# Performance work log

Hardware: AMD Instinct MI355X
Metric: run time of the kernel (lower is better)

The kernel has to match this reference:

```python
import jax, jax.numpy as jnp
import numpy as np

NEG = -1e9


def setup_inputs() -> dict:
    key = jax.random.key(0)
    kq, kk, kv, ke = jax.random.split(key, 4)
    B, H, S, D = 4, 16, 2048, 64
    q = jax.random.normal(kq, (B, H, S, D), dtype=jnp.float32)
    k = jax.random.normal(kk, (B, H, S, D), dtype=jnp.float32)
    v = jax.random.normal(kv, (B, H, S, D), dtype=jnp.float32)
    event_length = jax.random.randint(ke, (B,), 0, S, dtype=jnp.int32)
    return {"q": q, "k": k, "v": v, "event_length": event_length}


def reference(q, k, v, event_length):
    B, H, S, D = q.shape
    scale = jnp.sqrt(jnp.asarray(D, dtype=jnp.float32))
    # [b,h,s,q] scores
    scores = jnp.einsum('bhsd,bhqd->bhsq', q, k) / scale
    idx = jnp.arange(S)
    el = event_length[:, None]  # [B,1]
    valid = idx[None, :] < el   # [B,S]
    # mask[b,s,q] = valid[b,s] & valid[b,q]; broadcast over heads
    mask = (valid[:, None, :, None] & valid[:, None, None, :])  # [B,1,S,S]
    scores = jnp.where(mask, scores, NEG)
    attn = jax.nn.softmax(scores, axis=-1)
    # dropout p=0.0 (eval): identity
    out = jnp.einsum('bhsq,bhqd->bhsd', attn, v)
    return out
```

## Files before the change

kernel.cpp:

```cpp
#include <hip/hip_runtime.h>
#include <hip/hip_bf16.h>


#define SQ 2048
#define DH 64
#define NBH 64
#define TK 64
#define NTILE 32
#define TILE_B 8192
#define LDE 72
#define LVP 68

typedef __attribute__((ext_vector_type(4))) float f32x4;
typedef __attribute__((ext_vector_type(8))) short bf16x8;
typedef __attribute__((ext_vector_type(4))) unsigned int u32x4;
typedef __attribute__((ext_vector_type(2))) unsigned int u32x2;

__device__ __forceinline__ unsigned int pk2(float lo, float hi) {
    __hip_bfloat162 h = __float22bfloat162_rn(float2{lo, hi});
    union { __hip_bfloat162 h; unsigned int u; } c; c.h = h;
    return c.u;
}

__device__ __forceinline__ float bfu16_to_f(unsigned short s) {
    union { unsigned int u; float f; } c; c.u = ((unsigned int)s) << 16;
    return c.f;
}


__global__ __launch_bounds__(256)
void convkv(const float* __restrict__ K, const float* __restrict__ V,
            const int* __restrict__ EL, float* __restrict__ MV,
            char* __restrict__ Kbt, char* __restrict__ Vbt) {
    const int bh = blockIdx.x >> 5;
    const int kt = blockIdx.x & 31;
    const int k0 = kt * TK;
    const int el = EL[bh >> 4];
    const int t = threadIdx.x;
    const int r  = t >> 2;
    const int dc = t & 3;

    __shared__ short LV[64][LVP];

    {
        const float* vp = V + ((size_t)bh * SQ + k0 + r) * DH + dc * 16;
        f32x4 a = *(const f32x4*)vp;
        f32x4 b = *(const f32x4*)(vp + 4);
        f32x4 c2 = *(const f32x4*)(vp + 8);
        f32x4 d2 = *(const f32x4*)(vp + 12);
        u32x4 w0, w1;
        w0[0] = pk2(a[0], a[1]);  w0[1] = pk2(a[2], a[3]);
        w0[2] = pk2(b[0], b[1]);  w0[3] = pk2(b[2], b[3]);
        w1[0] = pk2(c2[0], c2[1]); w1[1] = pk2(c2[2], c2[3]);
        w1[2] = pk2(d2[0], d2[1]); w1[3] = pk2(d2[2], d2[3]);
        *(u32x4*)&LV[r][dc * 16]     = w0;
        *(u32x4*)&LV[r][dc * 16 + 8] = w1;
    }

    if (k0 < el) {
        const float* kp = K + ((size_t)bh * SQ + k0 + r) * DH + dc * 16;
        f32x4 a = *(const f32x4*)kp;
        f32x4 b = *(const f32x4*)(kp + 4);
        f32x4 c2 = *(const f32x4*)(kp + 8);
        f32x4 d2 = *(const f32x4*)(kp + 12);
        u32x4 w0, w1;
        w0[0] = pk2(a[0], a[1]);  w0[1] = pk2(a[2], a[3]);
        w0[2] = pk2(b[0], b[1]);  w0[3] = pk2(b[2], b[3]);
        w1[0] = pk2(c2[0], c2[1]); w1[1] = pk2(c2[2], c2[3]);
        w1[2] = pk2(d2[0], d2[1]); w1[3] = pk2(d2[2], d2[3]);
        char* kb = Kbt + (size_t)(bh * NTILE + kt) * TILE_B;
        const int fi  = (r >> 4) * 2 + (dc >> 1);
        const int qd0 = (dc & 1) * 2;
        char* d0 = kb + fi * 1024 + qd0 * 256 + (r & 15) * 16;
        *(u32x4*)d0         = w0;
        *(u32x4*)(d0 + 256) = w1;
    }

    __syncthreads();

    const int dd  = t >> 2;
    const int seg = t & 3;
    float msum = 0.f;
    unsigned int wv[8];
    #pragma unroll
    for (int i = 0; i < 8; ++i) {
        const int pos = seg * 16 + 2 * i;
        const int key = (pos & ~31) | ((pos & 4) << 2) | ((pos & 24) >> 1) | (pos & 3);
        const unsigned short s0 = (unsigned short)LV[key][dd];
        const unsigned short s1 = (unsigned short)LV[key + 1][dd];
        msum += bfu16_to_f(s0) + bfu16_to_f(s1);
        wv[i] = (unsigned int)s0 | ((unsigned int)s1 << 16);
    }
    msum += __shfl_xor(msum, 1);
    msum += __shfl_xor(msum, 2);
    if (seg == 0) atomicAdd(&MV[bh * DH + dd], msum * (1.0f / (float)SQ));

    if (k0 < el) {
        char* vbb = Vbt + (size_t)(bh * NTILE + kt) * TILE_B;
        const int fi  = (seg >> 1) * 4 + (dd >> 4);
        const int qd0 = (seg & 1) * 2;
        char* d0 = vbb + fi * 1024 + qd0 * 256 + (dd & 15) * 16;
        u32x4 o0 = {wv[0], wv[1], wv[2], wv[3]};
        u32x4 o1 = {wv[4], wv[5], wv[6], wv[7]};
        *(u32x4*)d0         = o0;
        *(u32x4*)(d0 + 256) = o1;
    }
}

__global__ __launch_bounds__(256, 3)
void flash8(const float* __restrict__ Q, const int* __restrict__ EL,
            const float* __restrict__ MV, float* __restrict__ O,
            const char* __restrict__ Kbt, const char* __restrict__ Vbt,
            int* __restrict__ ticket) {
    const int t = threadIdx.x;

    {
        const int bh0 = blockIdx.x & (NBH - 1);
        const int qb0 = (blockIdx.x >> 6) * 128;
        const int el32b = (EL[bh0 >> 4] + 31) & ~31;
        if (qb0 + 127 >= el32b) {
            float* Op = O + (size_t)bh0 * SQ * DH;
            const int c16 = t & 15, r0 = t >> 4;
            f32x4 mv = *(const f32x4*)(MV + bh0 * DH + c16 * 4);
            #pragma unroll
            for (int i = 0; i < 8; ++i) {
                const int row = qb0 + r0 + i * 16;
                if (row >= el32b)
                    *(f32x4*)(Op + (size_t)row * DH + c16 * 4) = mv;
            }
        }
    }

    const int el0 = EL[0], el1 = EL[1], el2 = EL[2], el3 = EL[3];
    const int w0_ = (el0 + 31) >> 5, w1_ = (el1 + 31) >> 5;
    const int w2_ = (el2 + 31) >> 5, w3_ = (el3 + 31) >> 5;
    const int n0 = 16 * w0_, n1 = n0 + 16 * w1_, n2 = n1 + 16 * w2_;
    const int nvalid = n2 + 16 * w3_;

    const int lane = t & 63, qd = lane >> 4, c = lane & 15;
    const float sc = 0.125f * 1.44269504f;

    for (;;) {
        int mytk = 0;
        if (lane == 0) mytk = atomicAdd(ticket, 1);
        const int it = __shfl(mytk, 0);
        if (it >= nvalid) break;

        int b, u, wb, el;
        if      (it < n0) { b = 0; u = it;      wb = w0_; el = el0; }
        else if (it < n1) { b = 1; u = it - n0; wb = w1_; el = el1; }
        else if (it < n2) { b = 2; u = it - n1; wb = w2_; el = el2; }
        else              { b = 3; u = it - n2; wb = w3_; el = el3; }
        const int head  = u / wb;
        const int qt    = u - head * wb;
        const int bh    = b * 16 + head;
        const int qbase = qt * 32;

        const float* Qp = Q + (size_t)bh * SQ * DH;
        float*       Op = O + (size_t)bh * SQ * DH;
        const size_t tb = (size_t)bh * NTILE * TILE_B + (size_t)lane * 16;
        const char*  Kt = Kbt + tb;
        const char*  Vt = Vbt + tb;

        bf16x8 qf[2][2];
        #pragma unroll
        for (int nt = 0; nt < 2; ++nt) {
            const int row = qbase + nt * 16 + c;
            #pragma unroll
            for (int kc = 0; kc < 2; ++kc) {
                const float* p = Qp + (size_t)row * DH + kc * 32 + qd * 8;
                f32x4 a  = *(const f32x4*)p;
                f32x4 bq = *(const f32x4*)(p + 4);
                u32x4 f;
                f[0] = pk2(a[0] * sc, a[1] * sc);
                f[1] = pk2(a[2] * sc, a[3] * sc);
                f[2] = pk2(bq[0] * sc, bq[1] * sc);
                f[3] = pk2(bq[2] * sc, bq[3] * sc);
                qf[nt][kc] = *(bf16x8*)&f;
            }
        }

        float l_[2] = {0.f, 0.f};
        f32x4 oacc[4][2];
        #pragma unroll
        for (int dt = 0; dt < 4; ++dt) {
            oacc[dt][0] = (f32x4){0.f, 0.f, 0.f, 0.f};
            oacc[dt][1] = (f32x4){0.f, 0.f, 0.f, 0.f};
        }

        const int nkt = (el + TK - 1) >> 6;

        for (int kt = 0; kt < nkt; ++kt) {
            const char* kb = Kt + (size_t)kt * TILE_B;
            const char* vb = Vt + (size_t)kt * TILE_B;

            bf16x8 ka[8];
            #pragma unroll
            for (int i = 0; i < 8; ++i)
                ka[i] = *(const bf16x8*)(kb + i * 1024);
            bf16x8 va[8];
            #pragma unroll
            for (int i = 0; i < 8; ++i)
                va[i] = *(const bf16x8*)(vb + i * 1024);

            const int k0 = kt * TK;
            const bool straddle = (k0 + TK > el);

            u32x4 pw[2][2];
            #pragma unroll
            for (int mt = 0; mt < 4; ++mt) {
                f32x4 s0 = (f32x4){0.f, 0.f, 0.f, 0.f};
                s0 = __builtin_amdgcn_mfma_f32_16x16x32_bf16(ka[mt*2],   qf[0][0], s0, 0, 0, 0);
                s0 = __builtin_amdgcn_mfma_f32_16x16x32_bf16(ka[mt*2+1], qf[0][1], s0, 0, 0, 0);
                f32x4 s1 = (f32x4){0.f, 0.f, 0.f, 0.f};
                s1 = __builtin_amdgcn_mfma_f32_16x16x32_bf16(ka[mt*2],   qf[1][0], s1, 0, 0, 0);
                s1 = __builtin_amdgcn_mfma_f32_16x16x32_bf16(ka[mt*2+1], qf[1][1], s1, 0, 0, 0);

                if (straddle) {
                    #pragma unroll
                    for (int r = 0; r < 4; ++r)
                        if (k0 + mt * 16 + qd * 4 + r >= el) {
                            s0[r] = -1e30f;
                            s1[r] = -1e30f;
                        }
                }

                #pragma unroll
                for (int nt = 0; nt < 2; ++nt) {
                    const f32x4 s = nt ? s1 : s0;
                    const float p0 = __builtin_amdgcn_exp2f(s[0]);
                    const float p1 = __builtin_amdgcn_exp2f(s[1]);
                    const float p2 = __builtin_amdgcn_exp2f(s[2]);
                    const float p3 = __builtin_amdgcn_exp2f(s[3]);
                    l_[nt] += (p0 + p1) + (p2 + p3);
                    pw[nt][mt >> 1][(mt & 1) * 2]     = pk2(p0, p1);
                    pw[nt][mt >> 1][(mt & 1) * 2 + 1] = pk2(p2, p3);
                }
            }

            #pragma unroll
            for (int kc = 0; kc < 2; ++kc) {
                bf16x8 pb0 = *(bf16x8*)&pw[0][kc];
                bf16x8 pb1 = *(bf16x8*)&pw[1][kc];
                #pragma unroll
                for (int dt = 0; dt < 4; ++dt) {
                    bf16x8 vf = va[kc * 4 + dt];
                    oacc[dt][0] = __builtin_amdgcn_mfma_f32_16x16x32_bf16(vf, pb0, oacc[dt][0], 0, 0, 0);
                    oacc[dt][1] = __builtin_amdgcn_mfma_f32_16x16x32_bf16(vf, pb1, oacc[dt][1], 0, 0, 0);
                }
            }
        }

        #pragma unroll
        for (int nt = 0; nt < 2; ++nt) {
            l_[nt] += __shfl_xor(l_[nt], 16);
            l_[nt] += __shfl_xor(l_[nt], 32);
        }

        #pragma unroll
        for (int nt = 0; nt < 2; ++nt) {
            const int qrow = qbase + nt * 16 + c;
            if (qrow < el) {
                const float inv = 1.0f / l_[nt];
                #pragma unroll
                for (int dt = 0; dt < 4; ++dt) {
                    f32x4 o = oacc[dt][nt];
                    o[0] *= inv; o[1] *= inv; o[2] *= inv; o[3] *= inv;
                    *(f32x4*)(Op + (size_t)qrow * DH + dt * 16 + qd * 4) = o;
                }
            } else {
                #pragma unroll
                for (int dt = 0; dt < 4; ++dt)
                    *(f32x4*)(Op + (size_t)qrow * DH + dt * 16 + qd * 4) =
                        *(const f32x4*)(MV + bh * DH + dt * 16 + qd * 4);
            }
        }
    }
}


__global__ __launch_bounds__(256)
void meanv_k(const float* __restrict__ V, float* __restrict__ MV) {
    const int bh  = blockIdx.x >> 4;
    const int seg = blockIdx.x & 15;
    const float* vp = V + ((size_t)bh * SQ + (size_t)seg * 128) * DH;
    const int c = threadIdx.x & 15;
    const int r = threadIdx.x >> 4;
    const float* p = vp + (size_t)r * DH + c * 4;
    f32x4 s0 = *(const f32x4*)(p);
    f32x4 s1 = *(const f32x4*)(p + 16 * DH);
    f32x4 s2 = *(const f32x4*)(p + 32 * DH);
    f32x4 s3 = *(const f32x4*)(p + 48 * DH);
    s0 += *(const f32x4*)(p + 64 * DH);
    s1 += *(const f32x4*)(p + 80 * DH);
    s2 += *(const f32x4*)(p + 96 * DH);
    s3 += *(const f32x4*)(p + 112 * DH);
    f32x4 s = (s0 + s1) + (s2 + s3);
    __shared__ f32x4 red[16][16];
    red[r][c] = s;
    __syncthreads();
    if (threadIdx.x < 16) {
        f32x4 a = red[0][threadIdx.x];
        #pragma unroll
        for (int j = 1; j < 16; ++j) a += red[j][threadIdx.x];
        const float inv = 1.0f / (float)SQ;
        atomicAdd(&MV[bh * DH + threadIdx.x * 4 + 0], a[0] * inv);
        atomicAdd(&MV[bh * DH + threadIdx.x * 4 + 1], a[1] * inv);
        atomicAdd(&MV[bh * DH + threadIdx.x * 4 + 2], a[2] * inv);
        atomicAdd(&MV[bh * DH + threadIdx.x * 4 + 3], a[3] * inv);
    }
}

__global__ __launch_bounds__(256, 3)
void flash5(const float* __restrict__ Q, const float* __restrict__ K,
            const float* __restrict__ V, const int* __restrict__ EL,
            const float* __restrict__ MV, float* __restrict__ O,
            int* __restrict__ ticket) {
    const int t = threadIdx.x;
    {
        const int bh0    = blockIdx.x & (NBH - 1);
        const int qbase0 = (blockIdx.x >> 6) * 128;
        const int elb    = EL[bh0 >> 4];
        if (qbase0 >= elb) {
            float* Op = O + (size_t)bh0 * SQ * DH;
            const int c16 = t & 15, r0 = t >> 4;
            f32x4 mv = *(const f32x4*)(MV + bh0 * DH + c16 * 4);
            #pragma unroll
            for (int i = 0; i < 8; ++i)
                *(f32x4*)(Op + (size_t)(qbase0 + r0 + i * 16) * DH + c16 * 4) = mv;
        }
    }

    const int el0 = EL[0], el1 = EL[1], el2 = EL[2], el3 = EL[3];
    const int v0 = (el0 + 127) >> 7, v1 = (el1 + 127) >> 7;
    const int v2 = (el2 + 127) >> 7, v3 = (el3 + 127) >> 7;
    const int n0 = 16 * v0, n1 = n0 + 16 * v1, n2 = n1 + 16 * v2;
    const int nvalid = n2 + 16 * v3;

    __shared__ short Kb[TK][LDE];
    __shared__ short Vt[DH][LDE];
    __shared__ short Pl[4][32][LDE];
    __shared__ int item_s;

    const int wq = t >> 6, lane = t & 63, qd = lane >> 4, c = lane & 15;
    const int ksrow = t >> 2;
    const int ksdc  = t & 3;
    const int vpair = t & 31;
    const int vdg   = t >> 5;

    for (;;) {
        if (t == 0) item_s = atomicAdd(ticket, 1);
        __syncthreads();
        const int it = item_s;
        if (it >= nvalid) break;

        int b, u, vb, el;
        if      (it < n0) { b = 0; u = it;      vb = v0; el = el0; }
        else if (it < n1) { b = 1; u = it - n0; vb = v1; el = el1; }
        else if (it < n2) { b = 2; u = it - n1; vb = v2; el = el2; }
        else              { b = 3; u = it - n2; vb = v3; el = el3; }
        const int head  = u / vb;
        const int qt    = u - head * vb;
        const int bh    = b * 16 + head;
        const int qbase = qt * 128;

        const size_t base = (size_t)bh * SQ * DH;
        const float* Qp = Q + base;
        const float* Kp = K + base;
        const float* Vp = V + base;
        float* Op = O + base;

        const float sc = 0.125f * 1.44269504f;
        bf16x8 qf[2][2];
        #pragma unroll
        for (int nt = 0; nt < 2; ++nt) {
            const int row = qbase + wq * 32 + nt * 16 + c;
            #pragma unroll
            for (int kc = 0; kc < 2; ++kc) {
                const float* p = Qp + (size_t)row * DH + kc * 32 + qd * 8;
                f32x4 a  = *(const f32x4*)p;
                f32x4 bb = *(const f32x4*)(p + 4);
                u32x4 f;
                f[0] = pk2(a[0] * sc, a[1] * sc);
                f[1] = pk2(a[2] * sc, a[3] * sc);
                f[2] = pk2(bb[0] * sc, bb[1] * sc);
                f[3] = pk2(bb[2] * sc, bb[3] * sc);
                qf[nt][kc] = *(bf16x8*)&f;
            }
        }

        float l_[2] = {0.f, 0.f};
        f32x4 oacc[4][2];
        #pragma unroll
        for (int dt = 0; dt < 4; ++dt)
            #pragma unroll
            for (int nt = 0; nt < 2; ++nt)
                oacc[dt][nt] = (f32x4){0.f, 0.f, 0.f, 0.f};

        const int nkt = (el + TK - 1) / TK;

        f32x4 kg0, kg1, kg2, kg3, vg0, vg1, vg2, vg3;
        {
            const float* kp = Kp + (size_t)ksrow * DH + ksdc * 16;
            kg0 = *(const f32x4*)kp;
            kg1 = *(const f32x4*)(kp + 4);
            kg2 = *(const f32x4*)(kp + 8);
            kg3 = *(const f32x4*)(kp + 12);
            const float* vp0 = Vp + (size_t)(2 * vpair) * DH + vdg * 8;
            vg0 = *(const f32x4*)vp0;
            vg1 = *(const f32x4*)(vp0 + 4);
            vg2 = *(const f32x4*)(vp0 + DH);
            vg3 = *(const f32x4*)(vp0 + DH + 4);
        }

        for (int kt = 0; kt < nkt; ++kt) {
            const int k0 = kt * TK;

            __syncthreads();
            {
                u32x4 w0, w1;
                w0[0] = pk2(kg0[0], kg0[1]); w0[1] = pk2(kg0[2], kg0[3]);
                w0[2] = pk2(kg1[0], kg1[1]); w0[3] = pk2(kg1[2], kg1[3]);
                w1[0] = pk2(kg2[0], kg2[1]); w1[1] = pk2(kg2[2], kg2[3]);
                w1[2] = pk2(kg3[0], kg3[1]); w1[3] = pk2(kg3[2], kg3[3]);
                *(u32x4*)&Kb[ksrow][ksdc * 16]     = w0;
                *(u32x4*)&Kb[ksrow][ksdc * 16 + 8] = w1;
            }
            {
                #pragma unroll
                for (int i = 0; i < 4; ++i) {
                    *(unsigned int*)&Vt[vdg * 8 + i][2 * vpair]     = pk2(vg0[i], vg2[i]);
                    *(unsigned int*)&Vt[vdg * 8 + 4 + i][2 * vpair] = pk2(vg1[i], vg3[i]);
                }
            }
            __syncthreads();

            if (kt + 1 < nkt) {
                const int kn = k0 + TK;
                const float* kp = Kp + (size_t)(kn + ksrow) * DH + ksdc * 16;
                kg0 = *(const f32x4*)kp;
                kg1 = *(const f32x4*)(kp + 4);
                kg2 = *(const f32x4*)(kp + 8);
                kg3 = *(const f32x4*)(kp + 12);
                const float* vp0 = Vp + (size_t)(kn + 2 * vpair) * DH + vdg * 8;
                vg0 = *(const f32x4*)vp0;
                vg1 = *(const f32x4*)(vp0 + 4);
                vg2 = *(const f32x4*)(vp0 + DH);
                vg3 = *(const f32x4*)(vp0 + DH + 4);
            }

            f32x4 st[4][2];
            #pragma unroll
            for (int mt = 0; mt < 4; ++mt) {
                bf16x8 a0 = *(const bf16x8*)&Kb[mt * 16 + c][qd * 8];
                bf16x8 a1 = *(const bf16x8*)&Kb[mt * 16 + c][32 + qd * 8];
                #pragma unroll
                for (int nt = 0; nt < 2; ++nt) {
                    f32x4 acc = (f32x4){0.f, 0.f, 0.f, 0.f};
                    acc = __builtin_amdgcn_mfma_f32_16x16x32_bf16(a0, qf[nt][0], acc, 0, 0, 0);
                    acc = __builtin_amdgcn_mfma_f32_16x16x32_bf16(a1, qf[nt][1], acc, 0, 0, 0);
                    st[mt][nt] = acc;
                }
            }

            if (k0 + TK > el) {
                #pragma unroll
                for (int mt = 0; mt < 4; ++mt)
                    #pragma unroll
                    for (int r = 0; r < 4; ++r)
                        if (k0 + mt * 16 + qd * 4 + r >= el) {
                            st[mt][0][r] = -1e30f;
                            st[mt][1][r] = -1e30f;
                        }
            }

            #pragma unroll
            for (int nt = 0; nt < 2; ++nt) {
                #pragma unroll
                for (int mt = 0; mt < 4; ++mt) {
                    const float p0 = exp2f(st[mt][nt][0]);
                    const float p1 = exp2f(st[mt][nt][1]);
                    const float p2 = exp2f(st[mt][nt][2]);
                    const float p3 = exp2f(st[mt][nt][3]);
                    l_[nt] += (p0 + p1) + (p2 + p3);
                    u32x2 pw;
                    pw[0] = pk2(p0, p1);
                    pw[1] = pk2(p2, p3);
                    *(u32x2*)&Pl[wq][nt * 16 + c][mt * 16 + qd * 4] = pw;
                }
            }

            #pragma unroll
            for (int kc = 0; kc < 2; ++kc) {
                bf16x8 pb0 = *(const bf16x8*)&Pl[wq][c][kc * 32 + qd * 8];
                bf16x8 pb1 = *(const bf16x8*)&Pl[wq][16 + c][kc * 32 + qd * 8];
                #pragma unroll
                for (int dt = 0; dt < 4; ++dt) {
                    bf16x8 vf = *(const bf16x8*)&Vt[dt * 16 + c][kc * 32 + qd * 8];
                    oacc[dt][0] = __builtin_amdgcn_mfma_f32_16x16x32_bf16(vf, pb0, oacc[dt][0], 0, 0, 0);
                    oacc[dt][1] = __builtin_amdgcn_mfma_f32_16x16x32_bf16(vf, pb1, oacc[dt][1], 0, 0, 0);
                }
            }
        }

        #pragma unroll
        for (int nt = 0; nt < 2; ++nt) {
            l_[nt] += __shfl_xor(l_[nt], 16);
            l_[nt] += __shfl_xor(l_[nt], 32);
        }

        #pragma unroll
        for (int nt = 0; nt < 2; ++nt) {
            const int row = qbase + wq * 32 + nt * 16 + c;
            if (row < el) {
                const float inv = 1.0f / l_[nt];
                #pragma unroll
                for (int dt = 0; dt < 4; ++dt) {
                    f32x4 o = oacc[dt][nt];
                    o[0] *= inv; o[1] *= inv; o[2] *= inv; o[3] *= inv;
                    *(f32x4*)(Op + (size_t)row * DH + dt * 16 + qd * 4) = o;
                }
            } else {
                #pragma unroll
                for (int dt = 0; dt < 4; ++dt) {
                    f32x4 mv = *(const f32x4*)(MV + bh * DH + dt * 16 + qd * 4);
                    *(f32x4*)(Op + (size_t)row * DH + dt * 16 + qd * 4) = mv;
                }
            }
        }
    }
}


extern "C" void kernel_launch(void* const* d_in, const int* in_sizes, int n_in,
                              void* d_out, int out_size, void* d_ws, size_t ws_size,
                              hipStream_t stream) {
    const float* q  = (const float*)d_in[0];
    const float* k  = (const float*)d_in[1];
    const float* v  = (const float*)d_in[2];
    const int*   el = (const int*)d_in[3];
    float* out = (float*)d_out;

    const size_t kbt_bytes = (size_t)NBH * NTILE * TILE_B;
    const size_t needed    = 65536 + 2 * kbt_bytes;

    if (ws_size >= needed) {
        float* mv  = (float*)d_ws;
        int*   tk  = (int*)((char*)d_ws + 16384);
        char*  kbt = (char*)d_ws + 65536;
        char*  vbt = kbt + kbt_bytes;

        hipMemsetAsync(d_ws, 0, 65536, stream);
        convkv<<<dim3(NBH * NTILE), dim3(256), 0, stream>>>(k, v, el, mv, kbt, vbt);
        flash8<<<dim3(NBH * (SQ / 128)), dim3(256), 0, stream>>>(q, el, mv, out, kbt, vbt, tk);
    } else {
        float* mv = (float*)d_ws;
        int*   tk = (int*)((char*)d_ws + NBH * DH * sizeof(float));

        hipMemsetAsync(d_ws, 0, NBH * DH * sizeof(float) + 64, stream);
        meanv_k<<<dim3(NBH * 16), dim3(256), 0, stream>>>(v, mv);
        flash5<<<dim3(NBH * (SQ / 128)), dim3(256), 0, stream>>>(q, k, v, el, mv, out, tk);
    }
}
```

Baseline: 210.4 us.

## Double-buffer K/V tile loads and shard work tickets into eight head groups

The K/V tile loop now uses two register buffers, issuing loads for tile kt+2 while tile kt is computed, so global loads overlap with MFMA and exp work. Work assignment splits the single atomic ticket into eight counters, one per head group selected by blockIdx, and sorts batches by event length so the longest work is handed out first. Launch bounds drop from 3 to 2 waves per SIMD to make room for the extra registers, which lowers occupancy.

```diff
diff --git a/kernel.cpp b/kernel.cpp
--- a/kernel.cpp
+++ b/kernel.cpp
@@ -107,11 +107,11 @@
     }
 }
 
-__global__ __launch_bounds__(256, 3)
-void flash8(const float* __restrict__ Q, const int* __restrict__ EL,
-            const float* __restrict__ MV, float* __restrict__ O,
-            const char* __restrict__ Kbt, const char* __restrict__ Vbt,
-            int* __restrict__ ticket) {
+__global__ __launch_bounds__(256, 2)
+void flash12(const float* __restrict__ Q, const int* __restrict__ EL,
+             const float* __restrict__ MV, float* __restrict__ O,
+             const char* __restrict__ Kbt, const char* __restrict__ Vbt,
+             int* __restrict__ ticket) {
     const int t = threadIdx.x;
 
     {
@@ -131,36 +131,47 @@
         }
     }
 
-    const int el0 = EL[0], el1 = EL[1], el2 = EL[2], el3 = EL[3];
-    const int w0_ = (el0 + 31) >> 5, w1_ = (el1 + 31) >> 5;
-    const int w2_ = (el2 + 31) >> 5, w3_ = (el3 + 31) >> 5;
-    const int n0 = 16 * w0_, n1 = n0 + 16 * w1_, n2 = n1 + 16 * w2_;
-    const int nvalid = n2 + 16 * w3_;
-
+    int ka0 = EL[0], va0 = 0;
+    int ka1 = EL[1], va1 = 1;
+    int ka2 = EL[2], va2 = 2;
+    int ka3 = EL[3], va3 = 3;
+    #define CSWAP(x, y) if (ka##x < ka##y) { int tk_ = ka##x, tv_ = va##x; \
+        ka##x = ka##y; va##x = va##y; ka##y = tk_; va##y = tv_; }
+    CSWAP(0, 1) CSWAP(2, 3) CSWAP(0, 2) CSWAP(1, 3) CSWAP(1, 2)
+    #undef CSWAP
+    const int c0 = 2 * ((ka0 + 31) >> 5);
+    const int c1 = 2 * ((ka1 + 31) >> 5);
+    const int c2 = 2 * ((ka2 + 31) >> 5);
+    const int c3 = 2 * ((ka3 + 31) >> 5);
+    const int nvalid = c0 + c1 + c2 + c3;
+
+    const int grp = blockIdx.x & 7;
     const int lane = t & 63, qd = lane >> 4, c = lane & 15;
     const float sc = 0.125f * 1.44269504f;
 
     for (;;) {
         int mytk = 0;
-        if (lane == 0) mytk = atomicAdd(ticket, 1);
+        if (lane == 0) mytk = atomicAdd(&ticket[grp], 1);
         const int it = __shfl(mytk, 0);
         if (it >= nvalid) break;
 
-        int b, u, wb, el;
-        if      (it < n0) { b = 0; u = it;      wb = w0_; el = el0; }
-        else if (it < n1) { b = 1; u = it - n0; wb = w1_; el = el1; }
-        else if (it < n2) { b = 2; u = it - n1; wb = w2_; el = el2; }
-        else              { b = 3; u = it - n2; wb = w3_; el = el3; }
-        const int head  = u / wb;
-        const int qt    = u - head * wb;
-        const int bh    = b * 16 + head;
+        int u = it, b, el;
+        if (u < c0)             { b = va0; el = ka0; }
+        else { u -= c0;
+        if (u < c1)             { b = va1; el = ka1; }
+        else { u -= c1;
+        if (u < c2)             { b = va2; el = ka2; }
+        else { u -= c2;           b = va3; el = ka3; } } }
+        const int vb_ = (el + 31) >> 5;
+        const int hh  = u / vb_;
+        const int qt  = u - hh * vb_;
+        const int bh  = b * 16 + grp + hh * 8;
         const int qbase = qt * 32;
 
         const float* Qp = Q + (size_t)bh * SQ * DH;
         float*       Op = O + (size_t)bh * SQ * DH;
-        const size_t tb = (size_t)bh * NTILE * TILE_B + (size_t)lane * 16;
-        const char*  Kt = Kbt + tb;
-        const char*  Vt = Vbt + tb;
+        const char*  Kt = Kbt + (size_t)bh * NTILE * TILE_B + (size_t)lane * 16;
+        const char*  Vt = Vbt + (size_t)bh * NTILE * TILE_B + (size_t)lane * 16;
 
         bf16x8 qf[2][2];
         #pragma unroll
@@ -190,66 +201,83 @@
 
         const int nkt = (el + TK - 1) >> 6;
 
-        for (int kt = 0; kt < nkt; ++kt) {
-            const char* kb = Kt + (size_t)kt * TILE_B;
-            const char* vb = Vt + (size_t)kt * TILE_B;
-
-            bf16x8 ka[8];
-            #pragma unroll
-            for (int i = 0; i < 8; ++i)
-                ka[i] = *(const bf16x8*)(kb + i * 1024);
-            bf16x8 va[8];
-            #pragma unroll
-            for (int i = 0; i < 8; ++i)
-                va[i] = *(const bf16x8*)(vb + i * 1024);
-
-            const int k0 = kt * TK;
-            const bool straddle = (k0 + TK > el);
-
-            u32x4 pw[2][2];
-            #pragma unroll
-            for (int mt = 0; mt < 4; ++mt) {
-                f32x4 s0 = (f32x4){0.f, 0.f, 0.f, 0.f};
-                s0 = __builtin_amdgcn_mfma_f32_16x16x32_bf16(ka[mt*2],   qf[0][0], s0, 0, 0, 0);
-                s0 = __builtin_amdgcn_mfma_f32_16x16x32_bf16(ka[mt*2+1], qf[0][1], s0, 0, 0, 0);
-                f32x4 s1 = (f32x4){0.f, 0.f, 0.f, 0.f};
-                s1 = __builtin_amdgcn_mfma_f32_16x16x32_bf16(ka[mt*2],   qf[1][0], s1, 0, 0, 0);
-                s1 = __builtin_amdgcn_mfma_f32_16x16x32_bf16(ka[mt*2+1], qf[1][1], s1, 0, 0, 0);
-
-                if (straddle) {
-                    #pragma unroll
-                    for (int r = 0; r < 4; ++r)
-                        if (k0 + mt * 16 + qd * 4 + r >= el) {
-                            s0[r] = -1e30f;
-                            s1[r] = -1e30f;
-                        }
-                }
-
-                #pragma unroll
-                for (int nt = 0; nt < 2; ++nt) {
-                    const f32x4 s = nt ? s1 : s0;
-                    const float p0 = __builtin_amdgcn_exp2f(s[0]);
-                    const float p1 = __builtin_amdgcn_exp2f(s[1]);
-                    const float p2 = __builtin_amdgcn_exp2f(s[2]);
-                    const float p3 = __builtin_amdgcn_exp2f(s[3]);
-                    l_[nt] += (p0 + p1) + (p2 + p3);
-                    pw[nt][mt >> 1][(mt & 1) * 2]     = pk2(p0, p1);
-                    pw[nt][mt >> 1][(mt & 1) * 2 + 1] = pk2(p2, p3);
-                }
-            }
-
-            #pragma unroll
-            for (int kc = 0; kc < 2; ++kc) {
-                bf16x8 pb0 = *(bf16x8*)&pw[0][kc];
-                bf16x8 pb1 = *(bf16x8*)&pw[1][kc];
-                #pragma unroll
-                for (int dt = 0; dt < 4; ++dt) {
-                    bf16x8 vf = va[kc * 4 + dt];
-                    oacc[dt][0] = __builtin_amdgcn_mfma_f32_16x16x32_bf16(vf, pb0, oacc[dt][0], 0, 0, 0);
-                    oacc[dt][1] = __builtin_amdgcn_mfma_f32_16x16x32_bf16(vf, pb1, oacc[dt][1], 0, 0, 0);
-                }
-            }
-        }
+        bf16x8 kA[8], vA[8], kB[8], vB[8];
+
+        #define LOAD_TILE(KB_, VB_, kt_) {                                     \
+            const char* kb_ = Kt + (size_t)(kt_) * TILE_B;                     \
+            const char* vp_ = Vt + (size_t)(kt_) * TILE_B;                     \
+            _Pragma("unroll")                                                  \
+            for (int i_ = 0; i_ < 8; ++i_)                                     \
+                KB_[i_] = *(const bf16x8*)(kb_ + i_ * 1024);                   \
+            _Pragma("unroll")                                                  \
+            for (int i_ = 0; i_ < 8; ++i_)                                     \
+                VB_[i_] = *(const bf16x8*)(vp_ + i_ * 1024);                   \
+        }
+
+        #define COMPUTE_TILE(KB_, VB_, kt_) {                                  \
+            const int k0_ = (kt_) * TK;                                        \
+            const bool strad_ = (k0_ + TK > el);                               \
+            u32x4 pw_[2][2];                                                   \
+            _Pragma("unroll")                                                  \
+            for (int mt = 0; mt < 4; ++mt) {                                   \
+                f32x4 s0 = (f32x4){0.f, 0.f, 0.f, 0.f};                        \
+                s0 = __builtin_amdgcn_mfma_f32_16x16x32_bf16(KB_[mt*2],   qf[0][0], s0, 0, 0, 0); \
+                s0 = __builtin_amdgcn_mfma_f32_16x16x32_bf16(KB_[mt*2+1], qf[0][1], s0, 0, 0, 0); \
+                f32x4 s1 = (f32x4){0.f, 0.f, 0.f, 0.f};                        \
+                s1 = __builtin_amdgcn_mfma_f32_16x16x32_bf16(KB_[mt*2],   qf[1][0], s1, 0, 0, 0); \
+                s1 = __builtin_amdgcn_mfma_f32_16x16x32_bf16(KB_[mt*2+1], qf[1][1], s1, 0, 0, 0); \
+                if (strad_) {                                                  \
+                    _Pragma("unroll")                                          \
+                    for (int r_ = 0; r_ < 4; ++r_)                             \
+                        if (k0_ + mt * 16 + qd * 4 + r_ >= el) {               \
+                            s0[r_] = -1e30f;                                   \
+                            s1[r_] = -1e30f;                                   \
+                        }                                                      \
+                }                                                              \
+                {                                                              \
+                    const float p0 = __builtin_amdgcn_exp2f(s0[0]);            \
+                    const float p1 = __builtin_amdgcn_exp2f(s0[1]);            \
+                    const float p2 = __builtin_amdgcn_exp2f(s0[2]);            \
+                    const float p3 = __builtin_amdgcn_exp2f(s0[3]);            \
+                    l_[0] += (p0 + p1) + (p2 + p3);                            \
+                    pw_[0][mt >> 1][(mt & 1) * 2]     = pk2(p0, p1);           \
+                    pw_[0][mt >> 1][(mt & 1) * 2 + 1] = pk2(p2, p3);           \
+                }                                                              \
+                {                                                              \
+                    const float p0 = __builtin_amdgcn_exp2f(s1[0]);            \
+                    const float p1 = __builtin_amdgcn_exp2f(s1[1]);            \
+                    const float p2 = __builtin_amdgcn_exp2f(s1[2]);            \
+                    const float p3 = __builtin_amdgcn_exp2f(s1[3]);            \
+                    l_[1] += (p0 + p1) + (p2 + p3);                            \
+                    pw_[1][mt >> 1][(mt & 1) * 2]     = pk2(p0, p1);           \
+                    pw_[1][mt >> 1][(mt & 1) * 2 + 1] = pk2(p2, p3);           \
+                }                                                              \
+            }                                                                  \
+            _Pragma("unroll")                                                  \
+            for (int kc = 0; kc < 2; ++kc) {                                   \
+                bf16x8 pb0 = *(bf16x8*)&pw_[0][kc];                            \
+                bf16x8 pb1 = *(bf16x8*)&pw_[1][kc];                            \
+                _Pragma("unroll")                                              \
+                for (int dt = 0; dt < 4; ++dt) {                               \
+                    oacc[dt][0] = __builtin_amdgcn_mfma_f32_16x16x32_bf16(VB_[kc*4+dt], pb0, oacc[dt][0], 0, 0, 0); \
+                    oacc[dt][1] = __builtin_amdgcn_mfma_f32_16x16x32_bf16(VB_[kc*4+dt], pb1, oacc[dt][1], 0, 0, 0); \
+                }                                                              \
+            }                                                                  \
+        }
+
+        LOAD_TILE(kA, vA, 0)
+        if (nkt > 1) LOAD_TILE(kB, vB, 1)
+
+        for (int kt = 0; kt < nkt; kt += 2) {
+            COMPUTE_TILE(kA, vA, kt)
+            if (kt + 2 < nkt) LOAD_TILE(kA, vA, kt + 2)
+            if (kt + 1 >= nkt) break;
+            COMPUTE_TILE(kB, vB, kt + 1)
+            if (kt + 3 < nkt) LOAD_TILE(kB, vB, kt + 3)
+        }
+
+        #undef LOAD_TILE
+        #undef COMPUTE_TILE
 
         #pragma unroll
         for (int nt = 0; nt < 2; ++nt) {
@@ -552,7 +580,7 @@
 
         hipMemsetAsync(d_ws, 0, 65536, stream);
         convkv<<<dim3(NBH * NTILE), dim3(256), 0, stream>>>(k, v, el, mv, kbt, vbt);
-        flash8<<<dim3(NBH * (SQ / 128)), dim3(256), 0, stream>>>(q, el, mv, out, kbt, vbt, tk);
+        flash12<<<dim3(NBH * 16), dim3(256), 0, stream>>>(q, el, mv, out, kbt, vbt, tk);
     } else {
         float* mv = (float*)d_ws;
         int*   tk = (int*)((char*)d_ws + NBH * DH * sizeof(float));
```

After: 222.8 us. 5.9% more time.
